# Performance work log

Measured on AMD Instinct MI355X. Metric: run time of the kernel, lower is better.

## Reference

```python
import jax, jax.numpy as jnp
import numpy as np

DIM = 32            # per-head key/query dim
HEADS = 8
SCALES = (5,)
TOTAL = HEADS * DIM             # 256
QKV_CH = 3 * TOTAL              # 768
CAT_CH = QKV_CH * (1 + len(SCALES))   # 1536
PROJ_IN = TOTAL * (1 + len(SCALES))   # 512
ATT_EPS = 1e-15
BN_EPS = 1e-5


def _conv3d(x, w, groups=1, pad=0):
    return jax.lax.conv_general_dilated(
        x, w, window_strides=(1, 1, 1),
        padding=[(pad, pad)] * 3,
        dimension_numbers=('NCDHW', 'OIDHW', 'NCDHW'),
        feature_group_count=groups)


def setup_inputs() -> dict:
    key = jax.random.key(0)
    ks = jax.random.split(key, 9)
    B, C, D, H, W = 2, 256, 16, 32, 32
    C_out = 256
    x = jax.random.normal(ks[0], (B, C, D, H, W), jnp.float32)
    # qkv: 1x1x1 conv C -> 768, no bias, no norm/act
    w_qkv = jax.random.normal(ks[1], (QKV_CH, C, 1, 1, 1), jnp.float32) * (1.0 / np.sqrt(C))
    # aggreg scale=5: depthwise 5^3 conv (groups=768) + 1x1 grouped conv (groups=3*heads=24)
    w_dw = jax.random.normal(ks[2], (QKV_CH, 1, 5, 5, 5), jnp.float32) * (1.0 / np.sqrt(125))
    w_pw = jax.random.normal(ks[3], (QKV_CH, QKV_CH // (3 * HEADS), 1, 1, 1), jnp.float32) * (1.0 / np.sqrt(DIM))
    # proj: 1x1x1 conv 512 -> C_out, followed by BatchNorm3d (eval mode)
    w_proj = jax.random.normal(ks[4], (C_out, PROJ_IN, 1, 1, 1), jnp.float32) * (1.0 / np.sqrt(PROJ_IN))
    gamma = jax.random.normal(ks[5], (C_out,), jnp.float32) * 0.1 + 1.0
    beta = jax.random.normal(ks[6], (C_out,), jnp.float32) * 0.1
    rmean = jax.random.normal(ks[7], (C_out,), jnp.float32) * 0.1
    rvar = jax.random.uniform(ks[8], (C_out,), jnp.float32, 0.5, 1.5)
    return {'x': x, 'w_qkv': w_qkv, 'w_dw': w_dw, 'w_pw': w_pw,
            'w_proj': w_proj, 'gamma': gamma, 'beta': beta,
            'rmean': rmean, 'rvar': rvar}


def _relu_linear_att(qkv):
    # qkv: (B, CAT_CH, D, H, W)
    B, Cc, D, H, W = qkv.shape
    N = D * H * W
    h = Cc // (3 * DIM)  # effective heads = heads*(1+len(scales)) = 16
    qkv = qkv.reshape(B, h, 3 * DIM, N)
    q = jax.nn.relu(qkv[:, :, 0:DIM])          # (B,h,d,N)
    k = jax.nn.relu(qkv[:, :, DIM:2 * DIM])    # (B,h,d,N)
    v = qkv[:, :, 2 * DIM:]                    # (B,h,d,N)
    # pad v with a row of ones -> (B,h,d+1,N)
    v = jnp.concatenate([v, jnp.ones_like(v[:, :, :1])], axis=2)
    # vk = v @ k^T : (B,h,d+1,d) ; out = vk @ q : (B,h,d+1,N)
    vk = jnp.einsum('bhen,bhdn->bhed', v, k)
    out = jnp.einsum('bhed,bhdn->bhen', vk, q)
    out = out[:, :, :-1] / (out[:, :, -1:] + ATT_EPS)
    return out.reshape(B, h * DIM, D, H, W)


def reference(x, w_qkv, w_dw, w_pw, w_proj, gamma, beta, rmean, rvar):
    qkv = _conv3d(x, w_qkv)                                   # (B,768,D,H,W)
    agg = _conv3d(qkv, w_dw, groups=QKV_CH, pad=2)            # depthwise 5^3
    agg = _conv3d(agg, w_pw, groups=3 * HEADS)                # grouped 1x1
    cat = jnp.concatenate([qkv, agg], axis=1)                 # (B,1536,D,H,W)
    out = _relu_linear_att(cat)                               # (B,512,D,H,W)
    out = _conv3d(out, w_proj)                                # (B,C_out,D,H,W)
    # BatchNorm3d (inference): (x - mean)/sqrt(var+eps)*gamma + beta
    sh = (1, -1, 1, 1, 1)
    out = (out - rmean.reshape(sh)) * jax.lax.rsqrt(rvar.reshape(sh) + BN_EPS)
    out = out * gamma.reshape(sh) + beta.reshape(sh)
    return out
```

## Files before the change

### kernel.cpp

```cpp
#include <hip/hip_runtime.h>
#include <hip/hip_bf16.h>

constexpr int QKV  = 768;
constexpr int Nsp  = 16384;

typedef __attribute__((ext_vector_type(8))) short short8_t;
typedef __attribute__((ext_vector_type(4))) float f32x4;

__device__ inline unsigned short f2b(float f) {
    union { __hip_bfloat16 h; unsigned short u; } c;
    c.h = __float2bfloat16(f);
    return c.u;
}
__device__ inline float b2f(unsigned short u) {
    union { unsigned short u; __hip_bfloat16 h; } c;
    c.u = u;
    return __bfloat162float(c.h);
}
__device__ inline ushort4 f2b4(float4 v) {
    return make_ushort4(f2b(v.x), f2b(v.y), f2b(v.z), f2b(v.w));
}

__global__ __launch_bounds__(256)
void cvt_bf16(const float* __restrict__ in, unsigned short* __restrict__ out, int n4)
{
    int i = blockIdx.x * 256 + threadIdx.x;
    if (i < n4) {
        float4 v = reinterpret_cast<const float4*>(in)[i];
        reinterpret_cast<ushort4*>(out)[i] = f2b4(v);
    }
}

__global__ __launch_bounds__(256)
void transposeT(const float* __restrict__ in, size_t inBStride,
                unsigned short* __restrict__ out, int Cout, int cBase,
                int GRP, int hBase, const float* __restrict__ rden)
{
    const int n0 = blockIdx.x * 64;
    const int c0 = cBase + blockIdx.y * 64;
    const int b  = blockIdx.z;
    const float* inb = in + (size_t)b * inBStride;

    __shared__ float tl[64][66];
    const int t = threadIdx.x;

#pragma unroll
    for (int r = 0; r < 8; r++) {
        int id = t + 256 * r;
        int c  = id >> 5;
        int nh = id & 31;
        int cg = c0 + c;
        int inRow = ((cg >> 5) - hBase) * GRP + (cg & 31);
        float2 v = *reinterpret_cast<const float2*>(
            inb + (size_t)inRow * Nsp + n0 + nh * 2);
        if (rden) {
            float2 rv = *reinterpret_cast<const float2*>(
                rden + ((size_t)(b * 16 + (cg >> 5))) * Nsp + n0 + nh * 2);
            v.x = fmaxf(v.x, 0.f) * rv.x;
            v.y = fmaxf(v.y, 0.f) * rv.y;
        }
        tl[nh * 2 + 0][c] = v.x;
        tl[nh * 2 + 1][c] = v.y;
    }
    __syncthreads();

#pragma unroll
    for (int r = 0; r < 2; r++) {
        int id = t + 256 * r;
        int n  = id >> 3;
        int cq = id & 7;
        ushort4 lo = make_ushort4(f2b(tl[n][cq*8+0]), f2b(tl[n][cq*8+1]),
                                  f2b(tl[n][cq*8+2]), f2b(tl[n][cq*8+3]));
        ushort4 hi = make_ushort4(f2b(tl[n][cq*8+4]), f2b(tl[n][cq*8+5]),
                                  f2b(tl[n][cq*8+6]), f2b(tl[n][cq*8+7]));
        unsigned short* p = out + ((size_t)b * Nsp + n0 + n) * Cout + c0 + cq * 8;
        *reinterpret_cast<ushort4*>(p)     = lo;
        *reinterpret_cast<ushort4*>(p + 4) = hi;
    }
}

template<bool FUSE_BN>
__global__ __launch_bounds__(256)
void mfma_gemm(const unsigned short* __restrict__ A,
               const unsigned short* __restrict__ B,
               float* __restrict__ Y, int K, int M, size_t aBStride,
               const float* __restrict__ gamma, const float* __restrict__ beta,
               const float* __restrict__ rmean, const float* __restrict__ rvar)
{
    const int n0  = blockIdx.x * 128;
    const int co0 = blockIdx.y * 128;
    const int bz  = blockIdx.z;
    const int t   = threadIdx.x;

    __shared__ unsigned short a_lds[128][40];
    __shared__ unsigned short b_lds[128][40];

    const unsigned short* Ab = A + (size_t)bz * aBStride + (size_t)co0 * K;
    const unsigned short* Bb = B + ((size_t)bz * Nsp + n0) * K;

    const int lane = t & 63;
    const int wv   = t >> 6;
    const int wco  = wv >> 1;
    const int wn   = wv & 1;
    const int lr   = lane & 15;
    const int lg   = lane >> 4;

    f32x4 acc[4][4];
#pragma unroll
    for (int m = 0; m < 4; m++)
#pragma unroll
        for (int f = 0; f < 4; f++) acc[m][f] = (f32x4){0.f, 0.f, 0.f, 0.f};

    for (int k0 = 0; k0 < K; k0 += 32) {
        __syncthreads();
#pragma unroll
        for (int r = 0; r < 2; r++) {
            int id  = t + 256 * r;
            int row = id >> 2;
            int kq  = id & 3;
            *reinterpret_cast<int4*>(&a_lds[row][kq * 8]) =
                *reinterpret_cast<const int4*>(Ab + (size_t)row * K + k0 + kq * 8);
            *reinterpret_cast<int4*>(&b_lds[row][kq * 8]) =
                *reinterpret_cast<const int4*>(Bb + (size_t)row * K + k0 + kq * 8);
        }
        __syncthreads();

        short8_t af[4], bf[4];
#pragma unroll
        for (int m = 0; m < 4; m++)
            af[m] = *reinterpret_cast<const short8_t*>(&a_lds[wco * 64 + m * 16 + lr][lg * 8]);
#pragma unroll
        for (int f = 0; f < 4; f++)
            bf[f] = *reinterpret_cast<const short8_t*>(&b_lds[wn * 64 + f * 16 + lr][lg * 8]);
#pragma unroll
        for (int m = 0; m < 4; m++)
#pragma unroll
            for (int f = 0; f < 4; f++)
                acc[m][f] = __builtin_amdgcn_mfma_f32_16x16x32_bf16(
                    af[m], bf[f], acc[m][f], 0, 0, 0);
    }

#pragma unroll
    for (int m = 0; m < 4; m++) {
#pragma unroll
        for (int j = 0; j < 4; j++) {
            int co = co0 + wco * 64 + m * 16 + 4 * lg + j;
            float sc = 1.f, sh = 0.f;
            if (FUSE_BN) {
                float rs = rsqrtf(rvar[co] + 1e-5f);
                sc = gamma[co] * rs;
                sh = beta[co] - rmean[co] * sc;
            }
            float* yp = Y + ((size_t)bz * M + co) * Nsp + n0 + wn * 64 + lr;
#pragma unroll
            for (int f = 0; f < 4; f++) {
                float v = acc[m][f][j];
                yp[f * 16] = FUSE_BN ? fmaf(v, sc, sh) : v;
            }
        }
    }
}

#define FMA4(A, WV, R, K)                \
    A.x = fmaf(WV, R[K + 0], A.x);       \
    A.y = fmaf(WV, R[K + 1], A.y);       \
    A.z = fmaf(WV, R[K + 2], A.z);       \
    A.w = fmaf(WV, R[K + 3], A.w);

#define PLANE_STEP(Z, G0, G1, G2, G3, G4, DOWRITE, DOSTAGE)                   \
  {                                                                           \
    const int zz  = (Z);                                                      \
    const int cur = zz & 1;                                                   \
    __syncthreads();                                                          \
    float4 g = {0.f, 0.f, 0.f, 0.f};                                          \
    if (DOSTAGE)                                                              \
      g = *reinterpret_cast<const float4*>(Xc + (zz + 1) * 1024 +             \
                                           hrow * 32 + w4);                   \
    _Pragma("unroll")                                                         \
    for (int kh = 0; kh < 5; kh++) {                                          \
      const float* rp = &pl[cur][hrow + kh][w4];                              \
      float4 c0 = *reinterpret_cast<const float4*>(rp);                       \
      float4 c1 = *reinterpret_cast<const float4*>(rp + 4);                   \
      float r[8] = {c0.x, c0.y, c0.z, c0.w, c1.x, c1.y, c1.z, c1.w};          \
      _Pragma("unroll")                                                       \
      for (int kw = 0; kw < 5; kw++) {                                        \
        if (G0) { float wv = wr[  0 + kh * 5 + kw]; FMA4(a0, wv, r, kw) }     \
        if (G1) { float wv = wr[ 25 + kh * 5 + kw]; FMA4(a1, wv, r, kw) }     \
        if (G2) { float wv = wr[ 50 + kh * 5 + kw]; FMA4(a2, wv, r, kw) }     \
        if (G3) { float wv = wr[ 75 + kh * 5 + kw]; FMA4(a3, wv, r, kw) }     \
        if (G4) { float wv = wr[100 + kh * 5 + kw]; FMA4(a4, wv, r, kw) }     \
      }                                                                       \
    }                                                                         \
    if (DOWRITE)                                                              \
      *reinterpret_cast<ushort4*>(Yc + ((zz - 2) * 32 + hrow) * 32 + w4)      \
          = f2b4(a4);                                                         \
    a4 = a3; a3 = a2; a2 = a1; a1 = a0;                                       \
    a0.x = 0.f; a0.y = 0.f; a0.z = 0.f; a0.w = 0.f;                           \
    if (DOSTAGE) {                                                            \
      const int nxt = cur ^ 1;                                                \
      pl[nxt][hrow + 2][2 + w4 + 0] = g.x;                                    \
      pl[nxt][hrow + 2][2 + w4 + 1] = g.y;                                    \
      pl[nxt][hrow + 2][2 + w4 + 2] = g.z;                                    \
      pl[nxt][hrow + 2][2 + w4 + 3] = g.w;                                    \
    }                                                                         \
  }

__global__ __launch_bounds__(256)
void dwconv5(const float* __restrict__ X, const float* __restrict__ Wd,
             unsigned short* __restrict__ Y)
{
    const int ch = blockIdx.x;
    const int t  = threadIdx.x;

    __shared__ float pl[2][36][40];

    const float* Xc = X + (size_t)ch * Nsp;
    unsigned short* Yc = Y + (size_t)ch * Nsp;
    const float* wp = Wd + ch * 125;

    float wr[125];
#pragma unroll
    for (int i = 0; i < 125; i++) wr[i] = wp[i];

    for (int i = t; i < 2 * 36 * 40; i += 256)
        (&pl[0][0][0])[i] = 0.f;

    const int hrow = t >> 3;
    const int w4   = (t & 7) * 4;

    __syncthreads();
    {
        float4 g = *reinterpret_cast<const float4*>(Xc + hrow * 32 + w4);
        pl[0][hrow + 2][2 + w4 + 0] = g.x;
        pl[0][hrow + 2][2 + w4 + 1] = g.y;
        pl[0][hrow + 2][2 + w4 + 2] = g.z;
        pl[0][hrow + 2][2 + w4 + 3] = g.w;
    }

    float4 a0 = {0,0,0,0}, a1 = a0, a2 = a0, a3 = a0, a4 = a0;

    PLANE_STEP(0, true, true, true, false, false, false, true)
    PLANE_STEP(1, true, true, true, true,  false, false, true)
#pragma unroll 1
    for (int z = 2; z <= 13; z++) {
        PLANE_STEP(z, true, true, true, true, true, true, true)
    }
    PLANE_STEP(14, false, true,  true, true, true, true, true)
    PLANE_STEP(15, false, false, true, true, true, true, false)
    *reinterpret_cast<ushort4*>(Yc + ((14 * 32 + hrow) * 32 + w4)) = f2b4(a4);
    *reinterpret_cast<ushort4*>(Yc + ((15 * 32 + hrow) * 32 + w4)) = f2b4(a3);
}

__global__ __launch_bounds__(256)
void pwconv(const unsigned short* __restrict__ X, const float* __restrict__ Wp,
            float* __restrict__ Y)
{
    const int n0 = blockIdx.x * 256;
    const int g  = blockIdx.y;
    const int t  = threadIdx.x;
    const int lane = t & 63, wv = t >> 6;

    __shared__ float xs[32][256];

    const unsigned short* Xg = X + (size_t)(g * 32) * Nsp + n0;
#pragma unroll
    for (int rr = 0; rr < 8; rr++) {
        int r = wv + rr * 4;
        ushort4 u = *reinterpret_cast<const ushort4*>(Xg + (size_t)r * Nsp + lane * 4);
        float4 v = make_float4(b2f(u.x), b2f(u.y), b2f(u.z), b2f(u.w));
        *reinterpret_cast<float4*>(&xs[r][lane * 4]) = v;
    }
    __syncthreads();

    float xin[32];
#pragma unroll
    for (int j = 0; j < 32; j++) xin[j] = xs[j][t];

    const float* wg = Wp + g * 1024;
    float* Yg = Y + (size_t)(g * 32) * Nsp + n0;
#pragma unroll 4
    for (int co = 0; co < 32; co++) {
        float acc = 0;
#pragma unroll
        for (int j = 0; j < 32; j++) acc = fmaf(wg[co * 32 + j], xin[j], acc);
        Yg[(size_t)co * Nsp + t] = acc;
    }
}

__global__ __launch_bounds__(256)
void att_vk(const float* __restrict__ QKVb, const float* __restrict__ AGG2,
            float* __restrict__ vk_part)
{
    const int chunk = blockIdx.x;
    const int bh    = blockIdx.y;
    const int b = bh >> 4, head = bh & 15;
    const float* base = (head < 8)
        ? QKVb + ((size_t)b * QKV + head * 96) * Nsp
        : AGG2 + ((size_t)b * QKV + (head - 8) * 96) * Nsp;

    __shared__ float ks[32][256];
    __shared__ float vs[32][256];

    const int t = threadIdx.x;
    const int lane = t & 63, wv = t >> 6;
    const int a  = t & 15;
    const int e0 = t >> 4;
    const int d0 = 2 * a;
    const int rot = (2 * d0 + 34 * e0) & 255;

    float a00 = 0, a01 = 0, a10 = 0, a11 = 0, s0 = 0, s1 = 0;

    for (int sub = 0; sub < 4; sub++) {
        const int n0 = chunk * 1024 + sub * 256;
        __syncthreads();
#pragma unroll
        for (int rr = 0; rr < 16; rr++) {
            int rid = wv + rr * 4;
            if (rid < 32) {
                float4 v = *reinterpret_cast<const float4*>(
                    base + (size_t)(32 + rid) * Nsp + n0 + lane * 4);
                v.x = fmaxf(v.x, 0.f); v.y = fmaxf(v.y, 0.f);
                v.z = fmaxf(v.z, 0.f); v.w = fmaxf(v.w, 0.f);
                *reinterpret_cast<float4*>(&ks[rid][lane * 4]) = v;
            } else {
                float4 v = *reinterpret_cast<const float4*>(
                    base + (size_t)(64 + rid - 32) * Nsp + n0 + lane * 4);
                *reinterpret_cast<float4*>(&vs[rid - 32][lane * 4]) = v;
            }
        }
        __syncthreads();

#pragma unroll 4
        for (int n = 0; n < 256; n += 2) {
            int nn = (n + rot) & 255;
            float2 k0 = *reinterpret_cast<const float2*>(&ks[d0][nn]);
            float2 k1 = *reinterpret_cast<const float2*>(&ks[d0 + 1][nn]);
            float2 v0 = *reinterpret_cast<const float2*>(&vs[e0][nn]);
            float2 v1 = *reinterpret_cast<const float2*>(&vs[e0 + 16][nn]);
            a00 = fmaf(v0.x, k0.x, fmaf(v0.y, k0.y, a00));
            a01 = fmaf(v0.x, k1.x, fmaf(v0.y, k1.y, a01));
            a10 = fmaf(v1.x, k0.x, fmaf(v1.y, k0.y, a10));
            a11 = fmaf(v1.x, k1.x, fmaf(v1.y, k1.y, a11));
            s0 += k0.x + k0.y;
            s1 += k1.x + k1.y;
        }
    }

    float* vp = vk_part + ((size_t)bh * 16 + chunk) * 1056;
    vp[e0 * 32 + d0]            = a00;
    vp[e0 * 32 + d0 + 1]        = a01;
    vp[(e0 + 16) * 32 + d0]     = a10;
    vp[(e0 + 16) * 32 + d0 + 1] = a11;
    if (e0 == 0) {
        vp[32 * 32 + d0]     = s0;
        vp[32 * 32 + d0 + 1] = s1;
    }
}

__global__ __launch_bounds__(256)
void att_vk_reduce(const float* __restrict__ vk_part, float* __restrict__ vk)
{
    const int bh = blockIdx.x;
    const int t  = threadIdx.x;
    for (int id = t; id < 1056; id += 256) {
        const float* p = vk_part + (size_t)bh * 16 * 1056 + id;
        float s = 0;
#pragma unroll
        for (int c = 0; c < 16; c++) s += p[(size_t)c * 1056];
        vk[bh * 1056 + id] = s;
    }
}

__global__ __launch_bounds__(256)
void mprep(const float* __restrict__ Wproj, const float* __restrict__ vk,
           unsigned short* __restrict__ Mp)
{
    const int b   = blockIdx.y;
    const int co0 = blockIdx.x * 16;
    const int t   = threadIdx.x;
    for (int ci = 0; ci < 16; ci++) {
        int co = co0 + ci;
        for (int hd = t; hd < 512; hd += 256) {
            int h = hd >> 5, d = hd & 31;
            const float* wrow = Wproj + (size_t)co * 512 + h * 32;
            const float* vkb  = vk + (size_t)(b * 16 + h) * 1056 + d;
            float s = 0;
#pragma unroll
            for (int e = 0; e < 32; e++) s = fmaf(wrow[e], vkb[e * 32], s);
            Mp[((size_t)b * 256 + co) * 512 + hd] = f2b(s);
        }
    }
}

__global__ __launch_bounds__(256)
void rden_k(const float* __restrict__ QKVb, const float* __restrict__ AGG2,
            const float* __restrict__ vk, float* __restrict__ Rden)
{
    const int n0 = blockIdx.x * 256;
    const int bh = blockIdx.y;
    const int b = bh >> 4, head = bh & 15;
    const float* base = (head < 8)
        ? QKVb + ((size_t)b * QKV + head * 96) * Nsp
        : AGG2 + ((size_t)b * QKV + (head - 8) * 96) * Nsp;
    const float* vk1 = vk + (size_t)bh * 1056 + 1024;
    const int t = threadIdx.x;
    float acc = 0;
#pragma unroll
    for (int d = 0; d < 32; d++)
        acc = fmaf(vk1[d], fmaxf(base[(size_t)d * Nsp + n0 + t], 0.f), acc);
    Rden[(size_t)bh * Nsp + n0 + t] = 1.0f / (acc + 1e-15f);
}

extern "C" void kernel_launch(void* const* d_in, const int* in_sizes, int n_in,
                              void* d_out, int out_size, void* d_ws, size_t ws_size,
                              hipStream_t stream)
{
    const float* x      = (const float*)d_in[0];
    const float* w_qkv  = (const float*)d_in[1];
    const float* w_dw   = (const float*)d_in[2];
    const float* w_pw   = (const float*)d_in[3];
    const float* w_proj = (const float*)d_in[4];
    const float* gamma  = (const float*)d_in[5];
    const float* beta   = (const float*)d_in[6];
    const float* rmean  = (const float*)d_in[7];
    const float* rvar   = (const float*)d_in[8];
    float* out = (float*)d_out;

    const size_t SZ = (size_t)2 * QKV * Nsp * sizeof(float);
    const size_t RB = (size_t)2 * Nsp * 512 * sizeof(unsigned short);
    char* ws = (char*)d_ws;
    float* qkv  = (float*)ws;
    float* agg2 = (float*)(ws + SZ);
    char*  Rb   = ws + 2 * SZ;
    unsigned short* xT   = (unsigned short*)Rb;
    unsigned short* aggH = (unsigned short*)Rb;
    unsigned short* qT   = (unsigned short*)Rb;
    char* slab = Rb + RB;
    float* vkp  = (float*)slab;
    float* vkf  = vkp + (size_t)32 * 16 * 1056;
    float* rden = vkf + (size_t)32 * 1056;
    unsigned short* Mp  = (unsigned short*)(rden + (size_t)32 * 16384);
    unsigned short* wqb = Mp + (size_t)2 * 256 * 512;

    dim3 blk(256);
    cvt_bf16<<<dim3(192), blk, 0, stream>>>(w_qkv, wqb, 768 * 256 / 4);
    transposeT<<<dim3(256, 4, 2), blk, 0, stream>>>(
        x, (size_t)256 * Nsp, xT, 256, 0, 32, 0, nullptr);
    mfma_gemm<false><<<dim3(128, 6, 2), blk, 0, stream>>>(
        wqb, xT, qkv, 256, 768, 0, nullptr, nullptr, nullptr, nullptr);
    for (int b = 0; b < 2; b++) {
        dwconv5<<<dim3(768), blk, 0, stream>>>(
            qkv + (size_t)b * QKV * Nsp, w_dw, aggH);
        pwconv<<<dim3(64, 24), blk, 0, stream>>>(
            aggH, w_pw, agg2 + (size_t)b * QKV * Nsp);
    }
    att_vk<<<dim3(16, 32), blk, 0, stream>>>(qkv, agg2, vkp);
    att_vk_reduce<<<dim3(32), blk, 0, stream>>>(vkp, vkf);
    mprep<<<dim3(16, 2), blk, 0, stream>>>(w_proj, vkf, Mp);
    rden_k<<<dim3(64, 32), blk, 0, stream>>>(qkv, agg2, vkf, rden);
    transposeT<<<dim3(256, 4, 2), blk, 0, stream>>>(
        qkv, (size_t)QKV * Nsp, qT, 512, 0, 96, 0, rden);
    transposeT<<<dim3(256, 4, 2), blk, 0, stream>>>(
        agg2, (size_t)QKV * Nsp, qT, 512, 256, 96, 8, rden);
    mfma_gemm<true><<<dim3(128, 2, 2), blk, 0, stream>>>(
        Mp, qT, out, 512, 256, (size_t)256 * 512,
        gamma, beta, rmean, rvar);
}
```

Baseline: 403.1 us.

## Store qkv and aggregated intermediates in bf16 and merge per-batch conv launches

The QKV GEMM output and the pointwise-conv output now go to bf16 buffers instead of fp32, and every consumer (dwconv, att_vk, rden, transpose) reads bf16 and widens it to float. The goal is to halve memory traffic on the large 768x16384x2 intermediates. The per-batch loop over dwconv and pwconv becomes a single launch with a batch grid dimension. The trade is lower precision in the qkv and agg values that feed the attention sums.

```diff
diff --git a/kernel.cpp b/kernel.cpp
--- a/kernel.cpp
+++ b/kernel.cpp
@@ -5,6 +5,7 @@
 constexpr int Nsp  = 16384;
 
 typedef __attribute__((ext_vector_type(8))) short short8_t;
+typedef __attribute__((ext_vector_type(8))) unsigned short ushort8_t;
 typedef __attribute__((ext_vector_type(4))) float f32x4;
 
 __device__ inline unsigned short f2b(float f) {
@@ -13,9 +14,10 @@
     return c.u;
 }
 __device__ inline float b2f(unsigned short u) {
-    union { unsigned short u; __hip_bfloat16 h; } c;
-    c.u = u;
-    return __bfloat162float(c.h);
+    unsigned v = (unsigned)u << 16;
+    float f;
+    __builtin_memcpy(&f, &v, 4);
+    return f;
 }
 __device__ inline ushort4 f2b4(float4 v) {
     return make_ushort4(f2b(v.x), f2b(v.y), f2b(v.z), f2b(v.w));
@@ -31,15 +33,15 @@
     }
 }
 
-__global__ __launch_bounds__(256)
-void transposeT(const float* __restrict__ in, size_t inBStride,
+template<bool IN_BF16>
+__global__ __launch_bounds__(256)
+void transposeT(const void* __restrict__ in_, size_t inBStride,
                 unsigned short* __restrict__ out, int Cout, int cBase,
                 int GRP, int hBase, const float* __restrict__ rden)
 {
     const int n0 = blockIdx.x * 64;
     const int c0 = cBase + blockIdx.y * 64;
     const int b  = blockIdx.z;
-    const float* inb = in + (size_t)b * inBStride;
 
     __shared__ float tl[64][66];
     const int t = threadIdx.x;
@@ -51,8 +53,17 @@
         int nh = id & 31;
         int cg = c0 + c;
         int inRow = ((cg >> 5) - hBase) * GRP + (cg & 31);
-        float2 v = *reinterpret_cast<const float2*>(
-            inb + (size_t)inRow * Nsp + n0 + nh * 2);
+        float2 v;
+        if (IN_BF16) {
+            const unsigned short* inb = (const unsigned short*)in_ + (size_t)b * inBStride;
+            ushort2 u = *reinterpret_cast<const ushort2*>(
+                inb + (size_t)inRow * Nsp + n0 + nh * 2);
+            v.x = b2f(u.x); v.y = b2f(u.y);
+        } else {
+            const float* inb = (const float*)in_ + (size_t)b * inBStride;
+            v = *reinterpret_cast<const float2*>(
+                inb + (size_t)inRow * Nsp + n0 + nh * 2);
+        }
         if (rden) {
             float2 rv = *reinterpret_cast<const float2*>(
                 rden + ((size_t)(b * 16 + (cg >> 5))) * Nsp + n0 + nh * 2);
@@ -79,11 +90,11 @@
     }
 }
 
-template<bool FUSE_BN>
+template<bool FUSE_BN, bool OUT_BF16>
 __global__ __launch_bounds__(256)
 void mfma_gemm(const unsigned short* __restrict__ A,
                const unsigned short* __restrict__ B,
-               float* __restrict__ Y, int K, int M, size_t aBStride,
+               void* __restrict__ Yv, int K, int M, size_t aBStride,
                const float* __restrict__ gamma, const float* __restrict__ beta,
                const float* __restrict__ rmean, const float* __restrict__ rvar)
 {
@@ -151,11 +162,19 @@
                 sc = gamma[co] * rs;
                 sh = beta[co] - rmean[co] * sc;
             }
-            float* yp = Y + ((size_t)bz * M + co) * Nsp + n0 + wn * 64 + lr;
-#pragma unroll
-            for (int f = 0; f < 4; f++) {
-                float v = acc[m][f][j];
-                yp[f * 16] = FUSE_BN ? fmaf(v, sc, sh) : v;
+            if (OUT_BF16) {
+                unsigned short* yp = (unsigned short*)Yv +
+                    ((size_t)bz * M + co) * Nsp + n0 + wn * 64 + lr;
+#pragma unroll
+                for (int f = 0; f < 4; f++) yp[f * 16] = f2b(acc[m][f][j]);
+            } else {
+                float* yp = (float*)Yv +
+                    ((size_t)bz * M + co) * Nsp + n0 + wn * 64 + lr;
+#pragma unroll
+                for (int f = 0; f < 4; f++) {
+                    float v = acc[m][f][j];
+                    yp[f * 16] = FUSE_BN ? fmaf(v, sc, sh) : v;
+                }
             }
         }
     }
@@ -172,10 +191,10 @@
     const int zz  = (Z);                                                      \
     const int cur = zz & 1;                                                   \
     __syncthreads();                                                          \
-    float4 g = {0.f, 0.f, 0.f, 0.f};                                          \
+    ushort4 gu = make_ushort4(0, 0, 0, 0);                                    \
     if (DOSTAGE)                                                              \
-      g = *reinterpret_cast<const float4*>(Xc + (zz + 1) * 1024 +             \
-                                           hrow * 32 + w4);                   \
+      gu = *reinterpret_cast<const ushort4*>(Xc + (zz + 1) * 1024 +           \
+                                             hrow * 32 + w4);                 \
     _Pragma("unroll")                                                         \
     for (int kh = 0; kh < 5; kh++) {                                          \
       const float* rp = &pl[cur][hrow + kh][w4];                              \
@@ -198,24 +217,25 @@
     a0.x = 0.f; a0.y = 0.f; a0.z = 0.f; a0.w = 0.f;                           \
     if (DOSTAGE) {                                                            \
       const int nxt = cur ^ 1;                                                \
-      pl[nxt][hrow + 2][2 + w4 + 0] = g.x;                                    \
-      pl[nxt][hrow + 2][2 + w4 + 1] = g.y;                                    \
-      pl[nxt][hrow + 2][2 + w4 + 2] = g.z;                                    \
-      pl[nxt][hrow + 2][2 + w4 + 3] = g.w;                                    \
+      pl[nxt][hrow + 2][2 + w4 + 0] = b2f(gu.x);                              \
+      pl[nxt][hrow + 2][2 + w4 + 1] = b2f(gu.y);                              \
+      pl[nxt][hrow + 2][2 + w4 + 2] = b2f(gu.z);                              \
+      pl[nxt][hrow + 2][2 + w4 + 3] = b2f(gu.w);                              \
     }                                                                         \
   }
 
 __global__ __launch_bounds__(256)
-void dwconv5(const float* __restrict__ X, const float* __restrict__ Wd,
+void dwconv5(const unsigned short* __restrict__ X, const float* __restrict__ Wd,
              unsigned short* __restrict__ Y)
 {
     const int ch = blockIdx.x;
+    const int b  = blockIdx.y;
     const int t  = threadIdx.x;
 
     __shared__ float pl[2][36][40];
 
-    const float* Xc = X + (size_t)ch * Nsp;
-    unsigned short* Yc = Y + (size_t)ch * Nsp;
+    const unsigned short* Xc = X + ((size_t)b * QKV + ch) * Nsp;
+    unsigned short*       Yc = Y + ((size_t)b * QKV + ch) * Nsp;
     const float* wp = Wd + ch * 125;
 
     float wr[125];
@@ -230,11 +250,11 @@
 
     __syncthreads();
     {
-        float4 g = *reinterpret_cast<const float4*>(Xc + hrow * 32 + w4);
-        pl[0][hrow + 2][2 + w4 + 0] = g.x;
-        pl[0][hrow + 2][2 + w4 + 1] = g.y;
-        pl[0][hrow + 2][2 + w4 + 2] = g.z;
-        pl[0][hrow + 2][2 + w4 + 3] = g.w;
+        ushort4 gu = *reinterpret_cast<const ushort4*>(Xc + hrow * 32 + w4);
+        pl[0][hrow + 2][2 + w4 + 0] = b2f(gu.x);
+        pl[0][hrow + 2][2 + w4 + 1] = b2f(gu.y);
+        pl[0][hrow + 2][2 + w4 + 2] = b2f(gu.z);
+        pl[0][hrow + 2][2 + w4 + 3] = b2f(gu.w);
     }
 
     float4 a0 = {0,0,0,0}, a1 = a0, a2 = a0, a3 = a0, a4 = a0;
@@ -253,22 +273,25 @@
 
 __global__ __launch_bounds__(256)
 void pwconv(const unsigned short* __restrict__ X, const float* __restrict__ Wp,
-            float* __restrict__ Y)
+            unsigned short* __restrict__ Y)
 {
     const int n0 = blockIdx.x * 256;
     const int g  = blockIdx.y;
+    const int bz = blockIdx.z;
     const int t  = threadIdx.x;
     const int lane = t & 63, wv = t >> 6;
 
     __shared__ float xs[32][256];
 
-    const unsigned short* Xg = X + (size_t)(g * 32) * Nsp + n0;
+    const unsigned short* Xg = X + ((size_t)bz * QKV + g * 32) * Nsp + n0;
 #pragma unroll
     for (int rr = 0; rr < 8; rr++) {
         int r = wv + rr * 4;
         ushort4 u = *reinterpret_cast<const ushort4*>(Xg + (size_t)r * Nsp + lane * 4);
-        float4 v = make_float4(b2f(u.x), b2f(u.y), b2f(u.z), b2f(u.w));
-        *reinterpret_cast<float4*>(&xs[r][lane * 4]) = v;
+        xs[r][lane * 4 + 0] = b2f(u.x);
+        xs[r][lane * 4 + 1] = b2f(u.y);
+        xs[r][lane * 4 + 2] = b2f(u.z);
+        xs[r][lane * 4 + 3] = b2f(u.w);
     }
     __syncthreads();
 
@@ -277,24 +300,25 @@
     for (int j = 0; j < 32; j++) xin[j] = xs[j][t];
 
     const float* wg = Wp + g * 1024;
-    float* Yg = Y + (size_t)(g * 32) * Nsp + n0;
+    unsigned short* Yg = Y + ((size_t)bz * QKV + g * 32) * Nsp + n0;
 #pragma unroll 4
     for (int co = 0; co < 32; co++) {
         float acc = 0;
 #pragma unroll
         for (int j = 0; j < 32; j++) acc = fmaf(wg[co * 32 + j], xin[j], acc);
-        Yg[(size_t)co * Nsp + t] = acc;
-    }
-}
-
-__global__ __launch_bounds__(256)
-void att_vk(const float* __restrict__ QKVb, const float* __restrict__ AGG2,
+        Yg[(size_t)co * Nsp + t] = f2b(acc);
+    }
+}
+
+__global__ __launch_bounds__(256)
+void att_vk(const unsigned short* __restrict__ QKVb,
+            const unsigned short* __restrict__ AGG2,
             float* __restrict__ vk_part)
 {
     const int chunk = blockIdx.x;
     const int bh    = blockIdx.y;
     const int b = bh >> 4, head = bh & 15;
-    const float* base = (head < 8)
+    const unsigned short* base = (head < 8)
         ? QKVb + ((size_t)b * QKV + head * 96) * Nsp
         : AGG2 + ((size_t)b * QKV + (head - 8) * 96) * Nsp;
 
@@ -302,7 +326,6 @@
     __shared__ float vs[32][256];
 
     const int t = threadIdx.x;
-    const int lane = t & 63, wv = t >> 6;
     const int a  = t & 15;
     const int e0 = t >> 4;
     const int d0 = 2 * a;
@@ -314,18 +337,21 @@
         const int n0 = chunk * 1024 + sub * 256;
         __syncthreads();
 #pragma unroll
-        for (int rr = 0; rr < 16; rr++) {
-            int rid = wv + rr * 4;
+        for (int rr = 0; rr < 8; rr++) {
+            int id  = t + 256 * rr;
+            int rid = id >> 5;
+            int cg  = id & 31;
+            ushort8_t u = *reinterpret_cast<const ushort8_t*>(
+                base + (size_t)(32 + rid) * Nsp + n0 + cg * 8);
+            float f[8];
+#pragma unroll
+            for (int j = 0; j < 8; j++) f[j] = b2f(u[j]);
             if (rid < 32) {
-                float4 v = *reinterpret_cast<const float4*>(
-                    base + (size_t)(32 + rid) * Nsp + n0 + lane * 4);
-                v.x = fmaxf(v.x, 0.f); v.y = fmaxf(v.y, 0.f);
-                v.z = fmaxf(v.z, 0.f); v.w = fmaxf(v.w, 0.f);
-                *reinterpret_cast<float4*>(&ks[rid][lane * 4]) = v;
+#pragma unroll
+                for (int j = 0; j < 8; j++) ks[rid][cg * 8 + j] = fmaxf(f[j], 0.f);
             } else {
-                float4 v = *reinterpret_cast<const float4*>(
-                    base + (size_t)(64 + rid - 32) * Nsp + n0 + lane * 4);
-                *reinterpret_cast<float4*>(&vs[rid - 32][lane * 4]) = v;
+#pragma unroll
+                for (int j = 0; j < 8; j++) vs[rid - 32][cg * 8 + j] = f[j];
             }
         }
         __syncthreads();
@@ -393,13 +419,14 @@
 }
 
 __global__ __launch_bounds__(256)
-void rden_k(const float* __restrict__ QKVb, const float* __restrict__ AGG2,
+void rden_k(const unsigned short* __restrict__ QKVb,
+            const unsigned short* __restrict__ AGG2,
             const float* __restrict__ vk, float* __restrict__ Rden)
 {
     const int n0 = blockIdx.x * 256;
     const int bh = blockIdx.y;
     const int b = bh >> 4, head = bh & 15;
-    const float* base = (head < 8)
+    const unsigned short* base = (head < 8)
         ? QKVb + ((size_t)b * QKV + head * 96) * Nsp
         : AGG2 + ((size_t)b * QKV + (head - 8) * 96) * Nsp;
     const float* vk1 = vk + (size_t)bh * 1056 + 1024;
@@ -407,7 +434,7 @@
     float acc = 0;
 #pragma unroll
     for (int d = 0; d < 32; d++)
-        acc = fmaf(vk1[d], fmaxf(base[(size_t)d * Nsp + n0 + t], 0.f), acc);
+        acc = fmaf(vk1[d], fmaxf(b2f(base[(size_t)d * Nsp + n0 + t]), 0.f), acc);
     Rden[(size_t)bh * Nsp + n0 + t] = 1.0f / (acc + 1e-15f);
 }
 
@@ -426,17 +453,14 @@
     const float* rvar   = (const float*)d_in[8];
     float* out = (float*)d_out;
 
-    const size_t SZ = (size_t)2 * QKV * Nsp * sizeof(float);
-    const size_t RB = (size_t)2 * Nsp * 512 * sizeof(unsigned short);
-    char* ws = (char*)d_ws;
-    float* qkv  = (float*)ws;
-    float* agg2 = (float*)(ws + SZ);
-    char*  Rb   = ws + 2 * SZ;
-    unsigned short* xT   = (unsigned short*)Rb;
-    unsigned short* aggH = (unsigned short*)Rb;
-    unsigned short* qT   = (unsigned short*)Rb;
-    char* slab = Rb + RB;
-    float* vkp  = (float*)slab;
+    const size_t QB = (size_t)2 * QKV * Nsp;
+    unsigned short* qkv  = (unsigned short*)d_ws;
+    unsigned short* agg2 = qkv + QB;
+    unsigned short* Rb   = agg2 + QB;
+    unsigned short* xT   = Rb;
+    unsigned short* aggH = Rb;
+    unsigned short* qT   = Rb;
+    float* vkp  = (float*)(Rb + QB);
     float* vkf  = vkp + (size_t)32 * 16 * 1056;
     float* rden = vkf + (size_t)32 * 1056;
     unsigned short* Mp  = (unsigned short*)(rden + (size_t)32 * 16384);
@@ -444,25 +468,21 @@
 
     dim3 blk(256);
     cvt_bf16<<<dim3(192), blk, 0, stream>>>(w_qkv, wqb, 768 * 256 / 4);
-    transposeT<<<dim3(256, 4, 2), blk, 0, stream>>>(
+    transposeT<false><<<dim3(256, 4, 2), blk, 0, stream>>>(
         x, (size_t)256 * Nsp, xT, 256, 0, 32, 0, nullptr);
-    mfma_gemm<false><<<dim3(128, 6, 2), blk, 0, stream>>>(
+    mfma_gemm<false, true><<<dim3(128, 6, 2), blk, 0, stream>>>(
         wqb, xT, qkv, 256, 768, 0, nullptr, nullptr, nullptr, nullptr);
-    for (int b = 0; b < 2; b++) {
-        dwconv5<<<dim3(768), blk, 0, stream>>>(
-            qkv + (size_t)b * QKV * Nsp, w_dw, aggH);
-        pwconv<<<dim3(64, 24), blk, 0, stream>>>(
-            aggH, w_pw, agg2 + (size_t)b * QKV * Nsp);
-    }
+    dwconv5<<<dim3(768, 2), blk, 0, stream>>>(qkv, w_dw, aggH);
+    pwconv<<<dim3(64, 24, 2), blk, 0, stream>>>(aggH, w_pw, agg2);
     att_vk<<<dim3(16, 32), blk, 0, stream>>>(qkv, agg2, vkp);
     att_vk_reduce<<<dim3(32), blk, 0, stream>>>(vkp, vkf);
     mprep<<<dim3(16, 2), blk, 0, stream>>>(w_proj, vkf, Mp);
     rden_k<<<dim3(64, 32), blk, 0, stream>>>(qkv, agg2, vkf, rden);
-    transposeT<<<dim3(256, 4, 2), blk, 0, stream>>>(
+    transposeT<true><<<dim3(256, 4, 2), blk, 0, stream>>>(
         qkv, (size_t)QKV * Nsp, qT, 512, 0, 96, 0, rden);
-    transposeT<<<dim3(256, 4, 2), blk, 0, stream>>>(
+    transposeT<true><<<dim3(256, 4, 2), blk, 0, stream>>>(
         agg2, (size_t)QKV * Nsp, qT, 512, 256, 96, 8, rden);
-    mfma_gemm<true><<<dim3(128, 2, 2), blk, 0, stream>>>(
+    mfma_gemm<true, false><<<dim3(128, 2, 2), blk, 0, stream>>>(
         Mp, qT, out, 512, 256, (size_t)256 * 512,
         gamma, beta, rmean, rvar);
 }
```

New measurement: 363.0 us. 1.11x faster.
